# Performance work log

Hardware: AMD Instinct MI355X
Metric: run time of the kernel (lower is better)

## Reference

```python
import jax, jax.numpy as jnp
import numpy as np

NUM_HEADS = 16
HEAD_DIM = 128
QUERY_DIM = 2048
SCALE = HEAD_DIM ** -0.5


def setup_inputs() -> dict:
    key = jax.random.key(0)
    ks = jax.random.split(key, 11)
    B, L, D = 2, 2048, QUERY_DIM
    HD = NUM_HEADS * HEAD_DIM
    s = 0.02
    return {
        "x_q": jax.random.normal(ks[0], (B, L, D), jnp.float32),
        "x_k": jax.random.normal(ks[1], (B, L, D), jnp.float32),
        "x_v": jax.random.normal(ks[2], (B, L, D), jnp.float32),
        "Wq": jax.random.normal(ks[3], (D, HD), jnp.float32) * s,
        "bq": jnp.zeros((HD,), jnp.float32),
        "Wk": jax.random.normal(ks[4], (D, HD), jnp.float32) * s,
        "bk": jnp.zeros((HD,), jnp.float32),
        "Wv": jax.random.normal(ks[5], (D, HD), jnp.float32) * s,
        "bv": jnp.zeros((HD,), jnp.float32),
        "Wo": jax.random.normal(ks[6], (HD, D), jnp.float32) * s,
        "bo": jnp.zeros((D,), jnp.float32),
    }


def _split_heads(x):  # [b, l, h*d] -> [b, h, l, d]
    b, l, _ = x.shape
    return x.reshape(b, l, NUM_HEADS, HEAD_DIM).transpose(0, 2, 1, 3)


def reference(x_q, x_k, x_v, Wq, bq, Wk, bk, Wv, bv, Wo, bo):
    # Note: the torch module constructs norm_q/norm_k but NEVER applies them in forward.
    q = _split_heads(x_q @ Wq + bq)  # [b, h, l, d]
    k = _split_heads(x_k @ Wk + bk)
    v = _split_heads(x_v @ Wv + bv)
    scores = jnp.einsum("bhid,bhjd->bhij", q, k) * SCALE
    probs = jax.nn.softmax(scores, axis=-1)
    o = jnp.einsum("bhij,bhjd->bhid", probs, v)  # [b, h, l, d]
    b, h, l, d = o.shape
    o = o.transpose(0, 2, 1, 3).reshape(b, l, h * d)
    return o @ Wo + bo
```

## Files before the change

kernel.cpp:

```cpp
#include <hip/hip_runtime.h>


typedef _Float16 f16;
typedef __attribute__((ext_vector_type(8))) _Float16 f16x8;
typedef __attribute__((ext_vector_type(4))) _Float16 f16x4;
typedef __attribute__((ext_vector_type(4))) float f32x4;
typedef __attribute__((ext_vector_type(4))) unsigned int u32x4;

#define QSCALE (0.08838834764831845f * 1.4426950408889634f)
#define SWZ3(r) (((r) & 3) | (((r) >> 1) & 4))
#define SWZV(r) ((r) & 7)

static __device__ __forceinline__ void gload16(void* lds, const void* g) {
  __builtin_amdgcn_global_load_lds(
      (__attribute__((address_space(1))) void*)g,
      (__attribute__((address_space(3))) void*)lds, 16, 0, 0);
}

__global__ __launch_bounds__(256) void cvt_x_kernel(
    const float* __restrict__ x0, const float* __restrict__ x1,
    const float* __restrict__ x2, f16* __restrict__ out) {
  const float* x = blockIdx.z == 0 ? x0 : (blockIdx.z == 1 ? x1 : x2);
  f16* o = out + (size_t)blockIdx.z * 8388608;
  size_t i = ((size_t)blockIdx.x * 256 + threadIdx.x) * 8;
  f32x4 a = *(const f32x4*)(x + i);
  f32x4 b = *(const f32x4*)(x + i + 4);
  f16x8 r;
  r[0] = (f16)a[0]; r[1] = (f16)a[1]; r[2] = (f16)a[2]; r[3] = (f16)a[3];
  r[4] = (f16)b[0]; r[5] = (f16)b[1]; r[6] = (f16)b[2]; r[7] = (f16)b[3];
  *(f16x8*)(o + i) = r;
}

__global__ __launch_bounds__(256) void cvt_w_kernel(
    const float* __restrict__ w0, const float* __restrict__ w1,
    const float* __restrict__ w2, const float* __restrict__ w3,
    f16* __restrict__ out) {
  const float* W = blockIdx.z == 0 ? w0 : blockIdx.z == 1 ? w1
                 : blockIdx.z == 2 ? w2 : w3;
  f16* WT = out + (size_t)blockIdx.z * 4194304;
  __shared__ f16 tile[64][68];
  const int tx = threadIdx.x & 15, ty = threadIdx.x >> 4;
  const int k0 = blockIdx.y * 64, n0 = blockIdx.x * 64;
#pragma unroll
  for (int i = 0; i < 4; ++i) {
    int r = ty + i * 16;
    f32x4 v = *(const f32x4*)(W + (size_t)(k0 + r) * 2048 + n0 + tx * 4);
    tile[r][tx * 4 + 0] = (f16)v[0]; tile[r][tx * 4 + 1] = (f16)v[1];
    tile[r][tx * 4 + 2] = (f16)v[2]; tile[r][tx * 4 + 3] = (f16)v[3];
  }
  __syncthreads();
#pragma unroll
  for (int i = 0; i < 4; ++i) {
    int n = ty + i * 16;
    f16x4 o;
    o[0] = tile[tx * 4 + 0][n]; o[1] = tile[tx * 4 + 1][n];
    o[2] = tile[tx * 4 + 2][n]; o[3] = tile[tx * 4 + 3][n];
    *(f16x4*)(WT + (size_t)(n0 + n) * 2048 + k0 + tx * 4) = o;
  }
}

__global__ __launch_bounds__(512, 2) void gemm_qkv_kernel(
    const f16* __restrict__ Abase, const f16* __restrict__ Btbase,
    f16* __restrict__ Obase, const float* __restrict__ b0,
    const float* __restrict__ b1, const float* __restrict__ b2) {
  const int lid = blockIdx.x;
  const int logi = (lid & 7) * 48 + (lid >> 3);
  const int bn = logi & 7, bm = (logi >> 3) & 15, z = logi >> 7;
  const f16* A  = Abase  + (size_t)z * 8388608;
  const f16* Bt = Btbase + (size_t)z * 4194304;
  f16* Oz = Obase + (size_t)z * 8388608;
  const float* bias = z == 0 ? b0 : z == 1 ? b1 : b2;
  const float qsc = z == 0 ? QSCALE : 1.0f;
  const int tid = threadIdx.x, lane = tid & 63, w = tid >> 6;
  const int wm = w >> 2, wn = w & 3;
  const int l15 = lane & 15, lg = lane >> 4;
  __shared__ alignas(16) char smb[131072];

  f32x4 acc[8][4];
#pragma unroll
  for (int i = 0; i < 8; ++i)
#pragma unroll
    for (int j = 0; j < 4; ++j) acc[i][j] = (f32x4)0.f;

#define GSTAGE(KT, C_)                                                        \
  {                                                                           \
    char* Ab_ = smb + (C_) * 65536;                                           \
    char* Bb_ = Ab_ + 32768;                                                  \
    _Pragma("unroll") for (int p = 0; p < 4; ++p) {                           \
      int L = p * 8192 + tid * 16;                                            \
      int row = L >> 7, pcol = L & 127;                                       \
      int scol = pcol ^ ((row & 7) << 4);                                     \
      gload16(Ab_ + L,                                                        \
              (const char*)A + ((size_t)(bm * 256 + row) * 2048 + (KT) * 64) * 2 + scol); \
      gload16(Bb_ + L,                                                        \
              (const char*)Bt + ((size_t)(bn * 256 + row) * 2048 + (KT) * 64) * 2 + scol); \
    }                                                                         \
  }

#define GREADS(P)                                                             \
  _Pragma("unroll") for (int pp = 0; pp < 2; ++pp)                            \
    _Pragma("unroll") for (int h = 0; h < 2; ++h) {                           \
      int row = wm * 128 + ((P) * 2 + pp) * 16 + l15;                         \
      af[(P) & 1][pp][h] = *(const f16x8*)(                                   \
          Ab + row * 128 + ((h * 64 + lg * 16) ^ ((row & 7) << 4)));          \
    }

#define GMFMA(P)                                                              \
  __builtin_amdgcn_s_setprio(1);                                              \
  _Pragma("unroll") for (int pp = 0; pp < 2; ++pp)                            \
    _Pragma("unroll") for (int j = 0; j < 4; ++j)                             \
      _Pragma("unroll") for (int h = 0; h < 2; ++h)                           \
        acc[(P) * 2 + pp][j] = __builtin_amdgcn_mfma_f32_16x16x32_f16(        \
            af[(P) & 1][pp][h], bf[j][h], acc[(P) * 2 + pp][j], 0, 0, 0);     \
  __builtin_amdgcn_s_setprio(0);

  GSTAGE(0, 0);
#pragma unroll 1
  for (int kt = 0; kt < 32; ++kt) {
    const int c = kt & 1;
    if (kt < 31) {
      GSTAGE(kt + 1, c ^ 1);
      asm volatile("s_waitcnt vmcnt(8)" ::: "memory");
    } else {
      asm volatile("s_waitcnt vmcnt(0)" ::: "memory");
    }
    __builtin_amdgcn_s_barrier();

    const char* Ab = smb + c * 65536;
    const char* Bb = Ab + 32768;
    f16x8 af[2][2][2], bf[4][2];
    GREADS(0);
#pragma unroll
    for (int j = 0; j < 4; ++j)
#pragma unroll
      for (int h = 0; h < 2; ++h) {
        int row = wn * 64 + j * 16 + l15;
        bf[j][h] = *(const f16x8*)(Bb + row * 128 +
                                   ((h * 64 + lg * 16) ^ ((row & 7) << 4)));
      }
    asm volatile("s_waitcnt lgkmcnt(0)" ::: "memory");
    __builtin_amdgcn_sched_barrier(0);
    GMFMA(0);
    GREADS(1);
    __builtin_amdgcn_sched_barrier(0);
    __builtin_amdgcn_s_barrier();
    asm volatile("s_waitcnt lgkmcnt(0)" ::: "memory");
    __builtin_amdgcn_sched_barrier(0);
    GMFMA(1);
    GREADS(2);
    __builtin_amdgcn_sched_barrier(0);
    __builtin_amdgcn_s_barrier();
    asm volatile("s_waitcnt lgkmcnt(0)" ::: "memory");
    __builtin_amdgcn_sched_barrier(0);
    GMFMA(2);
    GREADS(3);
    __builtin_amdgcn_sched_barrier(0);
    __builtin_amdgcn_s_barrier();
    asm volatile("s_waitcnt lgkmcnt(0)" ::: "memory");
    __builtin_amdgcn_sched_barrier(0);
    GMFMA(3);
  }

#pragma unroll
  for (int i = 0; i < 8; ++i)
#pragma unroll
    for (int j = 0; j < 4; ++j) {
      int col = bn * 256 + wn * 64 + j * 16 + l15;
      int h = col >> 7, d = col & 127;
      float bv = bias[col];
#pragma unroll
      for (int r = 0; r < 4; ++r) {
        int rowg = bm * 256 + wm * 128 + i * 16 + lg * 4 + r;
        int b_ = rowg >> 11, lpos = rowg & 2047;
        Oz[(size_t)(b_ * 16 + h) * 262144 + (size_t)lpos * 128 + d] =
            (f16)((acc[i][j][r] + bv) * qsc);
      }
    }
#undef GSTAGE
#undef GREADS
#undef GMFMA
}

__global__ __launch_bounds__(256) void gemm_out_kernel(
    const f16* __restrict__ A, const f16* __restrict__ Bt,
    float* __restrict__ Out, const float* __restrict__ bias) {
  const int tid = threadIdx.x, lane = tid & 63, w = tid >> 6;
  const int wm = w >> 1, wn = w & 1;
  const int bm = blockIdx.y, bn = blockIdx.x;
  const int l15 = lane & 15, lg = lane >> 4;
  __shared__ alignas(16) f16 As[128 * 32];
  __shared__ alignas(16) f16 Bs[128 * 32];
  f32x4 acc[4][4];
#pragma unroll
  for (int i = 0; i < 4; ++i)
#pragma unroll
    for (int j = 0; j < 4; ++j) acc[i][j] = (f32x4)0.f;

  for (int kt = 0; kt < 64; ++kt) {
    __syncthreads();
#pragma unroll
    for (int i = 0; i < 2; ++i) {
      int c = i * 4 + w;
      int phys = c * 1024 + lane * 16;
      int row = phys >> 6, colb = phys & 63;
      gload16((char*)As + c * 1024,
              (const char*)A + ((size_t)(bm * 128 + row) * 2048 + kt * 32) * 2 + colb);
      gload16((char*)Bs + c * 1024,
              (const char*)Bt + ((size_t)(bn * 128 + row) * 2048 + kt * 32) * 2 + colb);
    }
    __syncthreads();
    f16x8 af[4], bf[4];
#pragma unroll
    for (int i = 0; i < 4; ++i)
      af[i] = *(const f16x8*)(As + (wm * 64 + i * 16 + l15) * 32 + lg * 8);
#pragma unroll
    for (int j = 0; j < 4; ++j)
      bf[j] = *(const f16x8*)(Bs + (wn * 64 + j * 16 + l15) * 32 + lg * 8);
#pragma unroll
    for (int i = 0; i < 4; ++i)
#pragma unroll
      for (int j = 0; j < 4; ++j)
        acc[i][j] = __builtin_amdgcn_mfma_f32_16x16x32_f16(af[i], bf[j], acc[i][j], 0, 0, 0);
  }
#pragma unroll
  for (int i = 0; i < 4; ++i)
#pragma unroll
    for (int j = 0; j < 4; ++j) {
      int col = bn * 128 + wn * 64 + j * 16 + l15;
      float bv = bias[col];
#pragma unroll
      for (int r = 0; r < 4; ++r) {
        int rowg = bm * 128 + wm * 64 + i * 16 + lg * 4 + r;
        Out[(size_t)rowg * 2048 + col] = acc[i][j][r] + bv;
      }
    }
}

__global__ __launch_bounds__(256) void tr_v_kernel(const f16* __restrict__ v,
                                                   f16* __restrict__ vtout) {
  const int bh = blockIdx.z;
  const f16* V = v + (size_t)bh * 262144;
  f16* VT = vtout + (size_t)bh * 262144;
  __shared__ f16 tile[64][68];
  const int tx = threadIdx.x & 15, ty = threadIdx.x >> 4;
  const int l0 = blockIdx.x * 64, d0 = blockIdx.y * 64;
#pragma unroll
  for (int i = 0; i < 4; ++i) {
    int r = ty + i * 16;
    f16x4 val = *(const f16x4*)(V + (size_t)(l0 + r) * 128 + d0 + tx * 4);
    tile[r][tx * 4 + 0] = val[0]; tile[r][tx * 4 + 1] = val[1];
    tile[r][tx * 4 + 2] = val[2]; tile[r][tx * 4 + 3] = val[3];
  }
  __syncthreads();
#pragma unroll
  for (int i = 0; i < 4; ++i) {
    int d = ty + i * 16;
    f16x4 o;
    o[0] = tile[tx * 4 + 0][d]; o[1] = tile[tx * 4 + 1][d];
    o[2] = tile[tx * 4 + 2][d]; o[3] = tile[tx * 4 + 3][d];
    *(f16x4*)(VT + (size_t)(d0 + d) * 2048 + l0 + tx * 4) = o;
  }
}

__global__ __launch_bounds__(512, 4) void attn_kernel(
    const f16* __restrict__ q, const f16* __restrict__ k,
    const f16* __restrict__ vt, f16* __restrict__ o) {
  const int orig = blockIdx.y * 16 + blockIdx.x;
  const int swz = (orig & 7) * 64 + (orig >> 3);
  const int qt = swz & 15, bh = swz >> 4;
  const int tid = threadIdx.x, lane = tid & 63, w = tid >> 6;
  const int l15 = lane & 15, lg = lane >> 4;
  const f16* Qb = q + (size_t)bh * 262144 + (size_t)qt * 128 * 128;
  const char* Kb = (const char*)(k + (size_t)bh * 262144);
  const char* Vtb = (const char*)(vt + (size_t)bh * 262144);
  __shared__ alignas(16) char sm[65536];

  f16x8 qf[4];
#pragma unroll
  for (int ks = 0; ks < 4; ++ks)
    qf[ks] = *(const f16x8*)(Qb + (w * 16 + l15) * 128 + ks * 32 + lg * 8);

  f32x4 oacc[8];
#pragma unroll
  for (int df = 0; df < 8; ++df) oacc[df] = (f32x4)0.f;
  float mrow = -1e30f, ps = 0.f;
  const int rA = ((l15 >> 2) << 3) + (l15 & 3);

#define STAGE(T, B)                                                          \
  {                                                                          \
    char* Ks_ = sm + (B) * 32768;                                            \
    char* Vs_ = Ks_ + 16384;                                                 \
    _Pragma("unroll") for (int i = 0; i < 2; ++i) {                          \
      int c = i * 8 + w;                                                     \
      int phys = c * 1024 + lane * 16;                                       \
      {                                                                      \
        int row = phys >> 8, pcol = phys & 255;                              \
        int lcol = pcol ^ (SWZ3(row) << 4);                                  \
        gload16(Ks_ + c * 1024, Kb + (size_t)((T) * 64 + row) * 256 + lcol); \
      }                                                                      \
      {                                                                      \
        int row = phys >> 7, pcol = phys & 127;                              \
        int lcol = pcol ^ (SWZV(row) << 4);                                  \
        gload16(Vs_ + c * 1024, Vtb + (size_t)row * 4096 + (T) * 128 + lcol);\
      }                                                                      \
    }                                                                        \
  }

  STAGE(0, 0);
  int cur = 0;
  for (int t = 0; t < 32; ++t) {
    __syncthreads();
    if (t < 31) STAGE(t + 1, cur ^ 1);
    const char* Ks = sm + cur * 32768;
    const char* Vs = Ks + 16384;

    f32x4 s[4];
#pragma unroll
    for (int nf = 0; nf < 4; ++nf) s[nf] = (f32x4)0.f;
    __builtin_amdgcn_s_setprio(1);
#pragma unroll
    for (int ks = 0; ks < 4; ++ks) {
      f16x8 kf[4];
#pragma unroll
      for (int nf = 0; nf < 4; ++nf) {
        int row = ((nf & 1) << 5) + ((nf >> 1) << 2) + rA;
        int colb = (ks * 64 + lg * 16) ^ (SWZ3(row) << 4);
        kf[nf] = *(const f16x8*)(Ks + row * 256 + colb);
      }
#pragma unroll
      for (int nf = 0; nf < 4; ++nf)
        s[nf] = __builtin_amdgcn_mfma_f32_16x16x32_f16(kf[nf], qf[ks], s[nf], 0, 0, 0);
    }
    __builtin_amdgcn_s_setprio(0);

    unsigned int pk[2][4];
    {
      float m0 = fmaxf(fmaxf(s[0][0], s[0][1]), fmaxf(s[0][2], s[0][3]));
      float m1 = fmaxf(fmaxf(s[1][0], s[1][1]), fmaxf(s[1][2], s[1][3]));
      float m2 = fmaxf(fmaxf(s[2][0], s[2][1]), fmaxf(s[2][2], s[2][3]));
      float m3 = fmaxf(fmaxf(s[3][0], s[3][1]), fmaxf(s[3][2], s[3][3]));
      float mx = fmaxf(fmaxf(m0, m1), fmaxf(m2, m3));
      mx = fmaxf(mx, __shfl_xor(mx, 16));
      mx = fmaxf(mx, __shfl_xor(mx, 32));
      if (!__all(mx <= mrow + 8.f)) {
        float mnew = fmaxf(mrow, mx);
        float sc = exp2f(mrow - mnew);
        mrow = mnew;
        ps *= sc;
#pragma unroll
        for (int r = 0; r < 4; ++r) {
          float scr = __shfl(sc, (lane & 48) | (lg * 4 + r));
#pragma unroll
          for (int df = 0; df < 8; ++df) oacc[df][r] *= scr;
        }
      }
      float m = mrow;
      float psum = 0.f;
#pragma unroll
      for (int nf = 0; nf < 4; ++nf)
#pragma unroll
        for (int h = 0; h < 2; ++h) {
          float p0 = exp2f(s[nf][2 * h] - m);
          float p1 = exp2f(s[nf][2 * h + 1] - m);
          psum += p0 + p1;
          pk[nf & 1][(nf >> 1) * 2 + h] =
              __builtin_bit_cast(unsigned int, __builtin_amdgcn_cvt_pkrtz(p0, p1));
        }
      ps += psum;
    }

    __builtin_amdgcn_s_setprio(1);
#pragma unroll
    for (int kvs = 0; kvs < 2; ++kvs) {
      f16x8 pa = __builtin_bit_cast(f16x8, *(const u32x4*)pk[kvs]);
#pragma unroll
      for (int df = 0; df < 8; ++df) {
        int row = df * 16 + l15;
        int colb = (kvs * 64 + lg * 16) ^ (SWZV(row) << 4);
        f16x8 vb = *(const f16x8*)(Vs + row * 128 + colb);
        oacc[df] = __builtin_amdgcn_mfma_f32_16x16x32_f16(pa, vb, oacc[df], 0, 0, 0);
      }
    }
    __builtin_amdgcn_s_setprio(0);
    cur ^= 1;
  }

  const int b_ = bh >> 4, h_ = bh & 15;
  f16* Ob = o + (size_t)b_ * 4194304 + (size_t)qt * 128 * 2048 + h_ * 128;
  float lr = ps;
  lr += __shfl_xor(lr, 16);
  lr += __shfl_xor(lr, 32);
  float inv = 1.f / lr;
#pragma unroll
  for (int r = 0; r < 4; ++r) {
    float invr = __shfl(inv, (lane & 48) | (lg * 4 + r));
    int rl = w * 16 + lg * 4 + r;
#pragma unroll
    for (int df = 0; df < 8; ++df)
      Ob[(size_t)rl * 2048 + df * 16 + l15] = (f16)(oacc[df][r] * invr);
  }
#undef STAGE
}

extern "C" void kernel_launch(void* const* d_in, const int* in_sizes, int n_in,
                              void* d_out, int out_size, void* d_ws, size_t ws_size,
                              hipStream_t stream) {
  const float* xq = (const float*)d_in[0];
  const float* xk = (const float*)d_in[1];
  const float* xv = (const float*)d_in[2];
  const float* Wq = (const float*)d_in[3];
  const float* bq = (const float*)d_in[4];
  const float* Wk = (const float*)d_in[5];
  const float* bk = (const float*)d_in[6];
  const float* Wv = (const float*)d_in[7];
  const float* bv = (const float*)d_in[8];
  const float* Wo = (const float*)d_in[9];
  const float* bo = (const float*)d_in[10];

  char* ws = (char*)d_ws;
  f16* xh   = (f16*)(ws);
  f16* wt   = (f16*)(ws + 50331648);
  f16* qkv  = (f16*)(ws + 83886080);
  f16* vtb  = (f16*)(ws);
  f16* oatt = (f16*)(ws + 16777216);
  float* outp = (float*)d_out;

  hipLaunchKernelGGL(cvt_x_kernel, dim3(4096, 1, 3), dim3(256), 0, stream,
                     xq, xk, xv, xh);
  hipLaunchKernelGGL(cvt_w_kernel, dim3(32, 32, 4), dim3(256), 0, stream,
                     Wq, Wk, Wv, Wo, wt);
  hipLaunchKernelGGL(gemm_qkv_kernel, dim3(384, 1, 1), dim3(512), 0, stream,
                     xh, wt, qkv, bq, bk, bv);
  hipLaunchKernelGGL(tr_v_kernel, dim3(32, 2, 32), dim3(256), 0, stream,
                     qkv + (size_t)2 * 8388608, vtb);
  hipLaunchKernelGGL(attn_kernel, dim3(16, 32), dim3(512), 0, stream,
                     qkv, qkv + (size_t)8388608, vtb, oatt);
  hipLaunchKernelGGL(gemm_out_kernel, dim3(16, 32), dim3(256), 0, stream,
                     oatt, wt + (size_t)3 * 4194304, outp, bo);
}
```

Before: 310.7 us.

## Unify QKV and output GEMMs into templated 128x256 pipelined kernel

The QKV GEMM tile shrinks from 256x256 to 128x256, which halves the accumulators and cuts LDS use to 96KB. The launch grid grows to 768 blocks so the work spreads more evenly across CUs. The output projection, previously a simple unpipelined 128x128 GEMM, now reuses the same double-buffered global_load_lds kernel with a 128x256 tile and 256 blocks. The smaller QKV tile costs some operand reuse and adds more global traffic.

```diff
diff --git a/kernel.cpp b/kernel.cpp
--- a/kernel.cpp
+++ b/kernel.cpp
@@ -59,59 +59,73 @@
   }
 }
 
-__global__ __launch_bounds__(512, 2) void gemm_qkv_kernel(
+template <int MODE>
+__global__ __launch_bounds__(512, 2) void gemm128_kernel(
     const f16* __restrict__ Abase, const f16* __restrict__ Btbase,
-    f16* __restrict__ Obase, const float* __restrict__ b0,
+    void* __restrict__ Obase, const float* __restrict__ b0,
     const float* __restrict__ b1, const float* __restrict__ b2) {
   const int lid = blockIdx.x;
-  const int logi = (lid & 7) * 48 + (lid >> 3);
-  const int bn = logi & 7, bm = (logi >> 3) & 15, z = logi >> 7;
+  int bn, bm, z;
+  if (MODE == 0) {
+    const int logi = (lid & 7) * 96 + (lid >> 3);
+    bn = logi & 7; bm = (logi >> 3) & 31; z = logi >> 8;
+  } else {
+    const int logi = (lid & 7) * 32 + (lid >> 3);
+    bn = logi & 7; bm = logi >> 3; z = 0;
+  }
   const f16* A  = Abase  + (size_t)z * 8388608;
   const f16* Bt = Btbase + (size_t)z * 4194304;
-  f16* Oz = Obase + (size_t)z * 8388608;
-  const float* bias = z == 0 ? b0 : z == 1 ? b1 : b2;
-  const float qsc = z == 0 ? QSCALE : 1.0f;
+  const float* bias = z == 0 ? b0 : (z == 1 ? b1 : b2);
+  const float qsc = (MODE == 0 && z == 0) ? QSCALE : 1.0f;
   const int tid = threadIdx.x, lane = tid & 63, w = tid >> 6;
   const int wm = w >> 2, wn = w & 3;
   const int l15 = lane & 15, lg = lane >> 4;
-  __shared__ alignas(16) char smb[131072];
-
-  f32x4 acc[8][4];
-#pragma unroll
-  for (int i = 0; i < 8; ++i)
+  __shared__ alignas(16) char smb[98304];
+
+  f32x4 acc[4][4];
+#pragma unroll
+  for (int i = 0; i < 4; ++i)
 #pragma unroll
     for (int j = 0; j < 4; ++j) acc[i][j] = (f32x4)0.f;
 
 #define GSTAGE(KT, C_)                                                        \
   {                                                                           \
-    char* Ab_ = smb + (C_) * 65536;                                           \
-    char* Bb_ = Ab_ + 32768;                                                  \
+    char* Ab_ = smb + (C_) * 49152;                                           \
+    char* Bb_ = Ab_ + 16384;                                                  \
+    _Pragma("unroll") for (int p = 0; p < 2; ++p) {                           \
+      int L = p * 8192 + tid * 16;                                            \
+      int row = L >> 7, pcol = L & 127;                                       \
+      int scol = pcol ^ ((row & 7) << 4);                                     \
+      gload16(Ab_ + L,                                                        \
+              (const char*)A + ((size_t)(bm * 128 + row) * 2048 + (KT) * 64) * 2 + scol); \
+    }                                                                         \
     _Pragma("unroll") for (int p = 0; p < 4; ++p) {                           \
       int L = p * 8192 + tid * 16;                                            \
       int row = L >> 7, pcol = L & 127;                                       \
       int scol = pcol ^ ((row & 7) << 4);                                     \
-      gload16(Ab_ + L,                                                        \
-              (const char*)A + ((size_t)(bm * 256 + row) * 2048 + (KT) * 64) * 2 + scol); \
       gload16(Bb_ + L,                                                        \
               (const char*)Bt + ((size_t)(bn * 256 + row) * 2048 + (KT) * 64) * 2 + scol); \
     }                                                                         \
   }
 
-#define GREADS(P)                                                             \
-  _Pragma("unroll") for (int pp = 0; pp < 2; ++pp)                            \
-    _Pragma("unroll") for (int h = 0; h < 2; ++h) {                           \
-      int row = wm * 128 + ((P) * 2 + pp) * 16 + l15;                         \
-      af[(P) & 1][pp][h] = *(const f16x8*)(                                   \
-          Ab + row * 128 + ((h * 64 + lg * 16) ^ ((row & 7) << 4)));          \
-    }
-
-#define GMFMA(P)                                                              \
+#define GREADS(H)                                                             \
+  _Pragma("unroll") for (int i = 0; i < 4; ++i) {                             \
+    int row = wm * 64 + i * 16 + l15;                                         \
+    af[H][i] = *(const f16x8*)(Ab + row * 128 +                               \
+                               (((H) * 64 + lg * 16) ^ ((row & 7) << 4)));    \
+  }                                                                           \
+  _Pragma("unroll") for (int j = 0; j < 4; ++j) {                             \
+    int row = wn * 64 + j * 16 + l15;                                         \
+    bf[H][j] = *(const f16x8*)(Bb + row * 128 +                               \
+                               (((H) * 64 + lg * 16) ^ ((row & 7) << 4)));    \
+  }
+
+#define GMFMA(H)                                                              \
   __builtin_amdgcn_s_setprio(1);                                              \
-  _Pragma("unroll") for (int pp = 0; pp < 2; ++pp)                            \
+  _Pragma("unroll") for (int i = 0; i < 4; ++i)                               \
     _Pragma("unroll") for (int j = 0; j < 4; ++j)                             \
-      _Pragma("unroll") for (int h = 0; h < 2; ++h)                           \
-        acc[(P) * 2 + pp][j] = __builtin_amdgcn_mfma_f32_16x16x32_f16(        \
-            af[(P) & 1][pp][h], bf[j][h], acc[(P) * 2 + pp][j], 0, 0, 0);     \
+      acc[i][j] = __builtin_amdgcn_mfma_f32_16x16x32_f16(                     \
+          af[H][i], bf[H][j], acc[i][j], 0, 0, 0);                            \
   __builtin_amdgcn_s_setprio(0);
 
   GSTAGE(0, 0);
@@ -120,24 +134,16 @@
     const int c = kt & 1;
     if (kt < 31) {
       GSTAGE(kt + 1, c ^ 1);
-      asm volatile("s_waitcnt vmcnt(8)" ::: "memory");
+      asm volatile("s_waitcnt vmcnt(6)" ::: "memory");
     } else {
       asm volatile("s_waitcnt vmcnt(0)" ::: "memory");
     }
     __builtin_amdgcn_s_barrier();
 
-    const char* Ab = smb + c * 65536;
-    const char* Bb = Ab + 32768;
-    f16x8 af[2][2][2], bf[4][2];
+    const char* Ab = smb + c * 49152;
+    const char* Bb = Ab + 16384;
+    f16x8 af[2][4], bf[2][4];
     GREADS(0);
-#pragma unroll
-    for (int j = 0; j < 4; ++j)
-#pragma unroll
-      for (int h = 0; h < 2; ++h) {
-        int row = wn * 64 + j * 16 + l15;
-        bf[j][h] = *(const f16x8*)(Bb + row * 128 +
-                                   ((h * 64 + lg * 16) ^ ((row & 7) << 4)));
-      }
     asm volatile("s_waitcnt lgkmcnt(0)" ::: "memory");
     __builtin_amdgcn_sched_barrier(0);
     GMFMA(0);
@@ -147,93 +153,43 @@
     asm volatile("s_waitcnt lgkmcnt(0)" ::: "memory");
     __builtin_amdgcn_sched_barrier(0);
     GMFMA(1);
-    GREADS(2);
-    __builtin_amdgcn_sched_barrier(0);
-    __builtin_amdgcn_s_barrier();
-    asm volatile("s_waitcnt lgkmcnt(0)" ::: "memory");
-    __builtin_amdgcn_sched_barrier(0);
-    GMFMA(2);
-    GREADS(3);
-    __builtin_amdgcn_sched_barrier(0);
-    __builtin_amdgcn_s_barrier();
-    asm volatile("s_waitcnt lgkmcnt(0)" ::: "memory");
-    __builtin_amdgcn_sched_barrier(0);
-    GMFMA(3);
-  }
-
-#pragma unroll
-  for (int i = 0; i < 8; ++i)
-#pragma unroll
-    for (int j = 0; j < 4; ++j) {
-      int col = bn * 256 + wn * 64 + j * 16 + l15;
-      int h = col >> 7, d = col & 127;
-      float bv = bias[col];
-#pragma unroll
-      for (int r = 0; r < 4; ++r) {
-        int rowg = bm * 256 + wm * 128 + i * 16 + lg * 4 + r;
-        int b_ = rowg >> 11, lpos = rowg & 2047;
-        Oz[(size_t)(b_ * 16 + h) * 262144 + (size_t)lpos * 128 + d] =
-            (f16)((acc[i][j][r] + bv) * qsc);
-      }
-    }
+  }
+
+  if (MODE == 0) {
+    f16* Oz = (f16*)Obase + (size_t)z * 8388608;
+#pragma unroll
+    for (int i = 0; i < 4; ++i)
+#pragma unroll
+      for (int j = 0; j < 4; ++j) {
+        int col = bn * 256 + wn * 64 + j * 16 + l15;
+        int h = col >> 7, d = col & 127;
+        float bv = bias[col];
+#pragma unroll
+        for (int r = 0; r < 4; ++r) {
+          int rowg = bm * 128 + wm * 64 + i * 16 + lg * 4 + r;
+          int b_ = rowg >> 11, lpos = rowg & 2047;
+          Oz[(size_t)(b_ * 16 + h) * 262144 + (size_t)lpos * 128 + d] =
+              (f16)((acc[i][j][r] + bv) * qsc);
+        }
+      }
+  } else {
+    float* Out = (float*)Obase;
+#pragma unroll
+    for (int i = 0; i < 4; ++i)
+#pragma unroll
+      for (int j = 0; j < 4; ++j) {
+        int col = bn * 256 + wn * 64 + j * 16 + l15;
+        float bv = bias[col];
+#pragma unroll
+        for (int r = 0; r < 4; ++r) {
+          int rowg = bm * 128 + wm * 64 + i * 16 + lg * 4 + r;
+          Out[(size_t)rowg * 2048 + col] = acc[i][j][r] + bv;
+        }
+      }
+  }
 #undef GSTAGE
 #undef GREADS
 #undef GMFMA
-}
-
-__global__ __launch_bounds__(256) void gemm_out_kernel(
-    const f16* __restrict__ A, const f16* __restrict__ Bt,
-    float* __restrict__ Out, const float* __restrict__ bias) {
-  const int tid = threadIdx.x, lane = tid & 63, w = tid >> 6;
-  const int wm = w >> 1, wn = w & 1;
-  const int bm = blockIdx.y, bn = blockIdx.x;
-  const int l15 = lane & 15, lg = lane >> 4;
-  __shared__ alignas(16) f16 As[128 * 32];
-  __shared__ alignas(16) f16 Bs[128 * 32];
-  f32x4 acc[4][4];
-#pragma unroll
-  for (int i = 0; i < 4; ++i)
-#pragma unroll
-    for (int j = 0; j < 4; ++j) acc[i][j] = (f32x4)0.f;
-
-  for (int kt = 0; kt < 64; ++kt) {
-    __syncthreads();
-#pragma unroll
-    for (int i = 0; i < 2; ++i) {
-      int c = i * 4 + w;
-      int phys = c * 1024 + lane * 16;
-      int row = phys >> 6, colb = phys & 63;
-      gload16((char*)As + c * 1024,
-              (const char*)A + ((size_t)(bm * 128 + row) * 2048 + kt * 32) * 2 + colb);
-      gload16((char*)Bs + c * 1024,
-              (const char*)Bt + ((size_t)(bn * 128 + row) * 2048 + kt * 32) * 2 + colb);
-    }
-    __syncthreads();
-    f16x8 af[4], bf[4];
-#pragma unroll
-    for (int i = 0; i < 4; ++i)
-      af[i] = *(const f16x8*)(As + (wm * 64 + i * 16 + l15) * 32 + lg * 8);
-#pragma unroll
-    for (int j = 0; j < 4; ++j)
-      bf[j] = *(const f16x8*)(Bs + (wn * 64 + j * 16 + l15) * 32 + lg * 8);
-#pragma unroll
-    for (int i = 0; i < 4; ++i)
-#pragma unroll
-      for (int j = 0; j < 4; ++j)
-        acc[i][j] = __builtin_amdgcn_mfma_f32_16x16x32_f16(af[i], bf[j], acc[i][j], 0, 0, 0);
-  }
-#pragma unroll
-  for (int i = 0; i < 4; ++i)
-#pragma unroll
-    for (int j = 0; j < 4; ++j) {
-      int col = bn * 128 + wn * 64 + j * 16 + l15;
-      float bv = bias[col];
-#pragma unroll
-      for (int r = 0; r < 4; ++r) {
-        int rowg = bm * 128 + wm * 64 + i * 16 + lg * 4 + r;
-        Out[(size_t)rowg * 2048 + col] = acc[i][j][r] + bv;
-      }
-    }
 }
 
 __global__ __launch_bounds__(256) void tr_v_kernel(const f16* __restrict__ v,
@@ -429,12 +385,12 @@
                      xq, xk, xv, xh);
   hipLaunchKernelGGL(cvt_w_kernel, dim3(32, 32, 4), dim3(256), 0, stream,
                      Wq, Wk, Wv, Wo, wt);
-  hipLaunchKernelGGL(gemm_qkv_kernel, dim3(384, 1, 1), dim3(512), 0, stream,
-                     xh, wt, qkv, bq, bk, bv);
+  hipLaunchKernelGGL((gemm128_kernel<0>), dim3(768), dim3(512), 0, stream,
+                     xh, wt, (void*)qkv, bq, bk, bv);
   hipLaunchKernelGGL(tr_v_kernel, dim3(32, 2, 32), dim3(256), 0, stream,
                      qkv + (size_t)2 * 8388608, vtb);
   hipLaunchKernelGGL(attn_kernel, dim3(16, 32), dim3(512), 0, stream,
                      qkv, qkv + (size_t)8388608, vtb, oatt);
-  hipLaunchKernelGGL(gemm_out_kernel, dim3(16, 32), dim3(256), 0, stream,
-                     oatt, wt + (size_t)3 * 4194304, outp, bo);
-}
+  hipLaunchKernelGGL((gemm128_kernel<1>), dim3(256), dim3(512), 0, stream,
+                     oatt, wt + (size_t)3 * 4194304, (void*)outp, bo, bo, bo);
+}
```

Result: faster. 291.9 us (-6.0%).
